# Kernel tuning notes

Measured on AMD Instinct MI355X. Metric: run time of the kernel, lower is better.

## Reference

```python
import jax, jax.numpy as jnp
import numpy as np

N = 16384
C = 128
F = 128

def setup_inputs() -> dict:
    key = jax.random.key(0)
    k1, k2, k3, k4 = jax.random.split(key, 4)
    X = jax.random.normal(k1, (N, C), dtype=jnp.float32)
    adj = jax.random.uniform(k2, (N, N), dtype=jnp.float32)
    W = jax.random.normal(k3, (C, F), dtype=jnp.float32) * 0.05
    b = jax.random.normal(k4, (F,), dtype=jnp.float32) * 0.05
    return {"X": X, "adj": adj, "W": W, "b": b}

def reference(X, adj, W, b):
    # adj_hat = adj + I (self-loops)
    adj_hat = adj + jnp.eye(adj.shape[0], dtype=adj.dtype)
    # D^{-1/2}: inverse of sqrt of the diagonal degree matrix == 1/sqrt(rowsum)
    d_inv_sqrt = 1.0 / jnp.sqrt(jnp.sum(adj_hat, axis=1))  # [N]
    # Symmetric normalization via row/col scaling (same math as D^-1/2 @ A @ D^-1/2)
    adj_norm = adj_hat * d_inv_sqrt[:, None] * d_inv_sqrt[None, :]
    # Feature transform first (N*C*F) then aggregate (N*N*F)
    out = adj_norm @ (X @ W) + b
    return jax.nn.relu(out)
```

## Files before the change

### kernel.cpp

```cpp
#include <hip/hip_runtime.h>
#include <hip/hip_bf16.h>

typedef __attribute__((ext_vector_type(8))) short short8;
typedef __attribute__((ext_vector_type(4))) float f32x4;

#define N_NODES 16384
#define FEAT 128

__device__ __forceinline__ short f2bf(float x) {
  union { float f; unsigned u; } v;
  v.f = x;
  unsigned r = v.u + 0x7fffu + ((v.u >> 16) & 1u);
  return (short)(r >> 16);
}

__global__ __launch_bounds__(256) void rowsum_kernel(
    const float* __restrict__ adj, float* __restrict__ dinv)
{
  const int row = blockIdx.x;
  const float4* p4 = (const float4*)(adj + (size_t)row * N_NODES);
  float s = 0.f;
  #pragma unroll 4
  for (int i = threadIdx.x; i < N_NODES / 4; i += 256) {
    float4 v = p4[i];
    s += (v.x + v.y) + (v.z + v.w);
  }
  #pragma unroll
  for (int off = 32; off > 0; off >>= 1) s += __shfl_down(s, off, 64);
  __shared__ float part[4];
  if ((threadIdx.x & 63) == 0) part[threadIdx.x >> 6] = s;
  __syncthreads();
  if (threadIdx.x == 0) {
    float tot = (part[0] + part[1]) + (part[2] + part[3]) + 1.0f;
    dinv[row] = rsqrtf(tot);
  }
}

__global__ __launch_bounds__(256) void xw_kernel(
    const float* __restrict__ X, const float* __restrict__ W,
    const float* __restrict__ dinv,
    __hip_bfloat16* __restrict__ Ynat, __hip_bfloat16* __restrict__ Ytg)
{
  __shared__ __align__(16) float Ws[64][128];
  __shared__ __align__(16) float Xs[32][128];
  __shared__ __align__(16) short Ts[128][40];
  const int tid = threadIdx.x;
  const int row0 = blockIdx.x << 5;

  {
    const float4* Xg = (const float4*)(X + ((size_t)row0 << 7));
    float4* Xl = (float4*)&Xs[0][0];
    #pragma unroll
    for (int i = 0; i < 4; ++i) Xl[tid + (i << 8)] = Xg[tid + (i << 8)];
  }
  const int f  = tid & 127;
  const int rr = tid >> 7;
  float acc[16];
  #pragma unroll
  for (int k = 0; k < 16; ++k) acc[k] = 0.f;

  for (int cc = 0; cc < 2; ++cc) {
    __syncthreads();
    {
      const float4* Wg = (const float4*)(W + ((size_t)cc << 13));
      float4* Wl = (float4*)&Ws[0][0];
      #pragma unroll
      for (int i = 0; i < 8; ++i) Wl[tid + (i << 8)] = Wg[tid + (i << 8)];
    }
    __syncthreads();
    for (int c4 = 0; c4 < 16; ++c4) {
      const int cl = c4 << 2;
      const float w0 = Ws[cl + 0][f];
      const float w1 = Ws[cl + 1][f];
      const float w2 = Ws[cl + 2][f];
      const float w3 = Ws[cl + 3][f];
      const int cg = (cc << 6) + cl;
      #pragma unroll
      for (int k = 0; k < 16; ++k) {
        const float4 x = *(const float4*)&Xs[rr + (k << 1)][cg];
        acc[k] += x.x * w0 + x.y * w1 + x.z * w2 + x.w * w3;
      }
    }
  }
  #pragma unroll
  for (int k = 0; k < 16; ++k) {
    const int r = rr + (k << 1);
    const float dv = dinv[row0 + r];
    const short v = f2bf(acc[k] * dv);
    ((short*)Ynat)[(size_t)(row0 + r) * FEAT + f] = v;
    Ts[f][r] = v;
  }
  __syncthreads();
  {
    const int f2 = tid >> 1;
    const int h  = (tid & 1) << 4;
    const short8 v0 = *(const short8*)&Ts[f2][h];
    const short8 v1 = *(const short8*)&Ts[f2][h + 8];
    short* o = (short*)Ytg + (size_t)f2 * N_NODES + row0 + h;
    *(short8*)(o)     = v0;
    *(short8*)(o + 8) = v1;
  }
}

__global__ __launch_bounds__(512) void spmm_kernel(
    const float* __restrict__ A,
    const __hip_bfloat16* __restrict__ Ynat,
    const __hip_bfloat16* __restrict__ Ytg,
    const float* __restrict__ dinv,
    const float* __restrict__ bias,
    float* __restrict__ out)
{
  __shared__ __align__(16) short As[2][64][72];
  __shared__ __align__(16) short Bs[2][128][72];
  const int tid  = threadIdx.x;
  const int row0 = blockIdx.x << 6;

  const int ar = tid >> 3;
  const int ak = (tid & 7) << 3;
  const float* Ag = A + (size_t)(row0 + ar) * N_NODES + ak;
  const int yf = tid >> 2;
  const int yk = (tid & 3) << 4;
  const short* Yg = (const short*)Ytg + (size_t)yf * N_NODES + yk;

  const int wid  = tid >> 6;
  const int wm   = wid >> 1;
  const int wf   = wid & 1;
  const int lane = tid & 63;
  const int lm   = lane & 15;
  const int lk   = (lane >> 4) << 3;

  f32x4 acc[4];
  #pragma unroll
  for (int c = 0; c < 4; ++c) acc[c] = (f32x4){0.f, 0.f, 0.f, 0.f};

  {
    const float4 a0 = *(const float4*)(Ag);
    const float4 a1 = *(const float4*)(Ag + 4);
    const short8 y0 = *(const short8*)(Yg);
    const short8 y1 = *(const short8*)(Yg + 8);
    short8 ac;
    ac[0] = f2bf(a0.x); ac[1] = f2bf(a0.y); ac[2] = f2bf(a0.z); ac[3] = f2bf(a0.w);
    ac[4] = f2bf(a1.x); ac[5] = f2bf(a1.y); ac[6] = f2bf(a1.z); ac[7] = f2bf(a1.w);
    *(short8*)&As[0][ar][ak]     = ac;
    *(short8*)&Bs[0][yf][yk]     = y0;
    *(short8*)&Bs[0][yf][yk + 8] = y1;
  }
  __syncthreads();

  int p = 0;
  for (int t = 0; t < N_NODES / 64; ++t) {
    float4 a0, a1; short8 y0, y1;
    const bool pre = (t + 1) < (N_NODES / 64);
    if (pre) {
      const float* Ab = Ag + ((size_t)(t + 1) << 6);
      a0 = *(const float4*)(Ab);
      a1 = *(const float4*)(Ab + 4);
      const short* Yb = Yg + ((t + 1) << 6);
      y0 = *(const short8*)(Yb);
      y1 = *(const short8*)(Yb + 8);
    }
    #pragma unroll
    for (int ks = 0; ks < 2; ++ks) {
      const short8 af = *(const short8*)&As[p][(wm << 4) + lm][(ks << 5) + lk];
      #pragma unroll
      for (int c = 0; c < 4; ++c) {
        const short8 bf = *(const short8*)&Bs[p][(wf << 6) + (c << 4) + lm][(ks << 5) + lk];
        acc[c] = __builtin_amdgcn_mfma_f32_16x16x32_bf16(af, bf, acc[c], 0, 0, 0);
      }
    }
    if (pre) {
      short8 ac;
      ac[0] = f2bf(a0.x); ac[1] = f2bf(a0.y); ac[2] = f2bf(a0.z); ac[3] = f2bf(a0.w);
      ac[4] = f2bf(a1.x); ac[5] = f2bf(a1.y); ac[6] = f2bf(a1.z); ac[7] = f2bf(a1.w);
      *(short8*)&As[p ^ 1][ar][ak]     = ac;
      *(short8*)&Bs[p ^ 1][yf][yk]     = y0;
      *(short8*)&Bs[p ^ 1][yf][yk + 8] = y1;
    }
    __syncthreads();
    p ^= 1;
  }

  const int lr = (lane >> 4) << 2;
  float dreg[4];
  #pragma unroll
  for (int r = 0; r < 4; ++r) dreg[r] = dinv[row0 + (wm << 4) + lr + r];
  #pragma unroll
  for (int c = 0; c < 4; ++c) {
    const int col = (wf << 6) + (c << 4) + lm;
    const float bv = bias[col];
    #pragma unroll
    for (int r = 0; r < 4; ++r) {
      const int row = row0 + (wm << 4) + lr + r;
      const float y = __bfloat162float(Ynat[(size_t)row * FEAT + col]);
      const float v = dreg[r] * (acc[c][r] + y) + bv;
      out[(size_t)row * FEAT + col] = v > 0.f ? v : 0.f;
    }
  }
}

extern "C" void kernel_launch(void* const* d_in, const int* in_sizes, int n_in,
                              void* d_out, int out_size, void* d_ws, size_t ws_size,
                              hipStream_t stream) {
  const float* X   = (const float*)d_in[0];
  const float* adj = (const float*)d_in[1];
  const float* W   = (const float*)d_in[2];
  const float* b   = (const float*)d_in[3];
  float* out = (float*)d_out;

  float* dinv = (float*)d_ws;
  __hip_bfloat16* Ynat = (__hip_bfloat16*)((char*)d_ws + (1 << 16));
  __hip_bfloat16* Ytg  = (__hip_bfloat16*)((char*)d_ws + (1 << 16) + (1 << 22));

  rowsum_kernel<<<N_NODES, 256, 0, stream>>>(adj, dinv);
  xw_kernel<<<N_NODES / 32, 256, 0, stream>>>(X, W, dinv, Ynat, Ytg);
  spmm_kernel<<<N_NODES / 64, 512, 0, stream>>>(adj, Ynat, Ytg, dinv, b, out);
}
```

Baseline: 478.0 us.

## Load Y fragments directly into registers from pre-packed layout, drop B LDS staging

xw_kernel now writes Y in a fragment-packed layout so each SpMM lane can load its MFMA B operands straight from global memory into registers, removing the Bs shared-memory tile and its LDS writes and reads. The SpMM loop is unrolled by two with ping-pong register buffers, A is prefetched two tiles ahead, and launch bounds request two blocks per CU. The cost is more registers per thread and duplicate global reads of Y across waves sharing the same wf, which L2 has to absorb.

Measured after the change: 487.4 us. Within noise of the previous version (+2.0%).

```diff
diff --git a/kernel.cpp b/kernel.cpp
--- a/kernel.cpp
+++ b/kernel.cpp
@@ -6,6 +6,7 @@
 
 #define N_NODES 16384
 #define FEAT 128
+#define NT 256
 
 __device__ __forceinline__ short f2bf(float x) {
   union { float f; unsigned u; } v;
@@ -39,7 +40,7 @@
 __global__ __launch_bounds__(256) void xw_kernel(
     const float* __restrict__ X, const float* __restrict__ W,
     const float* __restrict__ dinv,
-    __hip_bfloat16* __restrict__ Ynat, __hip_bfloat16* __restrict__ Ytg)
+    __hip_bfloat16* __restrict__ Ynat, __hip_bfloat16* __restrict__ Ypack)
 {
   __shared__ __align__(16) float Ws[64][128];
   __shared__ __align__(16) float Xs[32][128];
@@ -96,31 +97,69 @@
     const int h  = (tid & 1) << 4;
     const short8 v0 = *(const short8*)&Ts[f2][h];
     const short8 v1 = *(const short8*)&Ts[f2][h + 8];
-    short* o = (short*)Ytg + (size_t)f2 * N_NODES + row0 + h;
-    *(short8*)(o)     = v0;
-    *(short8*)(o + 8) = v1;
-  }
-}
-
-__global__ __launch_bounds__(512) void spmm_kernel(
+    short* o = (short*)Ypack;
+    *(short8*)(o + (size_t)(row0 + h) * FEAT + (f2 << 3))     = v0;
+    *(short8*)(o + (size_t)(row0 + h + 8) * FEAT + (f2 << 3)) = v1;
+  }
+}
+
+#define SPMM_BODY(T, BCUR, BNXT, ALD0, ALD1, AST0, AST1, RD, WR)               \
+  {                                                                            \
+    if ((T) + 2 < NT) {           \
+      const float* ap = Ag + (((T) + 2) << 6);                                 \
+      ALD0 = *(const float4*)(ap);                                             \
+      ALD1 = *(const float4*)(ap + 4);                                         \
+    }                                                                          \
+    if ((T) + 1 < NT) {  \
+      const short* yp0 = Yg + (((T) + 1) << 13);                               \
+      const short* yp1 = yp0 + 4096;                                           \
+      BNXT[0] = *(const short8*)(yp0);                                         \
+      BNXT[1] = *(const short8*)(yp0 + 128);                                   \
+      BNXT[2] = *(const short8*)(yp0 + 256);                                   \
+      BNXT[3] = *(const short8*)(yp0 + 384);                                   \
+      BNXT[4] = *(const short8*)(yp1);                                         \
+      BNXT[5] = *(const short8*)(yp1 + 128);                                   \
+      BNXT[6] = *(const short8*)(yp1 + 256);                                   \
+      BNXT[7] = *(const short8*)(yp1 + 384);                                   \
+    }                                                                          \
+    {                                                                          \
+      const short8 af0 = *(const short8*)&As[RD][(wm << 4) + lm][lk];          \
+      acc[0] = __builtin_amdgcn_mfma_f32_16x16x32_bf16(af0, BCUR[0], acc[0], 0, 0, 0); \
+      acc[1] = __builtin_amdgcn_mfma_f32_16x16x32_bf16(af0, BCUR[1], acc[1], 0, 0, 0); \
+      acc[2] = __builtin_amdgcn_mfma_f32_16x16x32_bf16(af0, BCUR[2], acc[2], 0, 0, 0); \
+      acc[3] = __builtin_amdgcn_mfma_f32_16x16x32_bf16(af0, BCUR[3], acc[3], 0, 0, 0); \
+      const short8 af1 = *(const short8*)&As[RD][(wm << 4) + lm][32 + lk];     \
+      acc[0] = __builtin_amdgcn_mfma_f32_16x16x32_bf16(af1, BCUR[4], acc[0], 0, 0, 0); \
+      acc[1] = __builtin_amdgcn_mfma_f32_16x16x32_bf16(af1, BCUR[5], acc[1], 0, 0, 0); \
+      acc[2] = __builtin_amdgcn_mfma_f32_16x16x32_bf16(af1, BCUR[6], acc[2], 0, 0, 0); \
+      acc[3] = __builtin_amdgcn_mfma_f32_16x16x32_bf16(af1, BCUR[7], acc[3], 0, 0, 0); \
+    }                                                                          \
+    if ((T) + 1 < NT) {  \
+      short8 ac;                                                               \
+      ac[0] = f2bf(AST0.x); ac[1] = f2bf(AST0.y);                              \
+      ac[2] = f2bf(AST0.z); ac[3] = f2bf(AST0.w);                              \
+      ac[4] = f2bf(AST1.x); ac[5] = f2bf(AST1.y);                              \
+      ac[6] = f2bf(AST1.z); ac[7] = f2bf(AST1.w);                              \
+      *(short8*)&As[WR][ar][ak] = ac;                                          \
+    }                                                                          \
+    __syncthreads();                                                           \
+  }
+
+__global__ __launch_bounds__(512, 2) void spmm_kernel(
     const float* __restrict__ A,
     const __hip_bfloat16* __restrict__ Ynat,
-    const __hip_bfloat16* __restrict__ Ytg,
+    const __hip_bfloat16* __restrict__ Ypack,
     const float* __restrict__ dinv,
     const float* __restrict__ bias,
     float* __restrict__ out)
 {
   __shared__ __align__(16) short As[2][64][72];
-  __shared__ __align__(16) short Bs[2][128][72];
   const int tid  = threadIdx.x;
   const int row0 = blockIdx.x << 6;
 
   const int ar = tid >> 3;
   const int ak = (tid & 7) << 3;
   const float* Ag = A + (size_t)(row0 + ar) * N_NODES + ak;
-  const int yf = tid >> 2;
-  const int yk = (tid & 3) << 4;
-  const short* Yg = (const short*)Ytg + (size_t)yf * N_NODES + yk;
 
   const int wid  = tid >> 6;
   const int wm   = wid >> 1;
@@ -129,55 +168,42 @@
   const int lm   = lane & 15;
   const int lk   = (lane >> 4) << 3;
 
+  const short* Yg = (const short*)Ypack + (lk << 7) + (wf << 9) + (lm << 3);
+
   f32x4 acc[4];
   #pragma unroll
   for (int c = 0; c < 4; ++c) acc[c] = (f32x4){0.f, 0.f, 0.f, 0.f};
 
-  {
-    const float4 a0 = *(const float4*)(Ag);
-    const float4 a1 = *(const float4*)(Ag + 4);
-    const short8 y0 = *(const short8*)(Yg);
-    const short8 y1 = *(const short8*)(Yg + 8);
+  float4 aA0, aA1, aB0, aB1;
+  short8 b0[8], b1[8];
+
+  aA0 = *(const float4*)(Ag);
+  aA1 = *(const float4*)(Ag + 4);
+  aB0 = *(const float4*)(Ag + 64);
+  aB1 = *(const float4*)(Ag + 68);
+  {
+    const short* yp0 = Yg;
+    const short* yp1 = Yg + 4096;
+    b0[0] = *(const short8*)(yp0);
+    b0[1] = *(const short8*)(yp0 + 128);
+    b0[2] = *(const short8*)(yp0 + 256);
+    b0[3] = *(const short8*)(yp0 + 384);
+    b0[4] = *(const short8*)(yp1);
+    b0[5] = *(const short8*)(yp1 + 128);
+    b0[6] = *(const short8*)(yp1 + 256);
+    b0[7] = *(const short8*)(yp1 + 384);
+  }
+  {
     short8 ac;
-    ac[0] = f2bf(a0.x); ac[1] = f2bf(a0.y); ac[2] = f2bf(a0.z); ac[3] = f2bf(a0.w);
-    ac[4] = f2bf(a1.x); ac[5] = f2bf(a1.y); ac[6] = f2bf(a1.z); ac[7] = f2bf(a1.w);
-    *(short8*)&As[0][ar][ak]     = ac;
-    *(short8*)&Bs[0][yf][yk]     = y0;
-    *(short8*)&Bs[0][yf][yk + 8] = y1;
+    ac[0] = f2bf(aA0.x); ac[1] = f2bf(aA0.y); ac[2] = f2bf(aA0.z); ac[3] = f2bf(aA0.w);
+    ac[4] = f2bf(aA1.x); ac[5] = f2bf(aA1.y); ac[6] = f2bf(aA1.z); ac[7] = f2bf(aA1.w);
+    *(short8*)&As[0][ar][ak] = ac;
   }
   __syncthreads();
 
-  int p = 0;
-  for (int t = 0; t < N_NODES / 64; ++t) {
-    float4 a0, a1; short8 y0, y1;
-    const bool pre = (t + 1) < (N_NODES / 64);
-    if (pre) {
-      const float* Ab = Ag + ((size_t)(t + 1) << 6);
-      a0 = *(const float4*)(Ab);
-      a1 = *(const float4*)(Ab + 4);
-      const short* Yb = Yg + ((t + 1) << 6);
-      y0 = *(const short8*)(Yb);
-      y1 = *(const short8*)(Yb + 8);
-    }
-    #pragma unroll
-    for (int ks = 0; ks < 2; ++ks) {
-      const short8 af = *(const short8*)&As[p][(wm << 4) + lm][(ks << 5) + lk];
-      #pragma unroll
-      for (int c = 0; c < 4; ++c) {
-        const short8 bf = *(const short8*)&Bs[p][(wf << 6) + (c << 4) + lm][(ks << 5) + lk];
-        acc[c] = __builtin_amdgcn_mfma_f32_16x16x32_bf16(af, bf, acc[c], 0, 0, 0);
-      }
-    }
-    if (pre) {
-      short8 ac;
-      ac[0] = f2bf(a0.x); ac[1] = f2bf(a0.y); ac[2] = f2bf(a0.z); ac[3] = f2bf(a0.w);
-      ac[4] = f2bf(a1.x); ac[5] = f2bf(a1.y); ac[6] = f2bf(a1.z); ac[7] = f2bf(a1.w);
-      *(short8*)&As[p ^ 1][ar][ak]     = ac;
-      *(short8*)&Bs[p ^ 1][yf][yk]     = y0;
-      *(short8*)&Bs[p ^ 1][yf][yk + 8] = y1;
-    }
-    __syncthreads();
-    p ^= 1;
+  for (int t = 0; t < NT; t += 2) {
+    SPMM_BODY(t,     b0, b1, aA0, aA1, aB0, aB1, 0, 1)
+    SPMM_BODY(t + 1, b1, b0, aB0, aB1, aA0, aA1, 1, 0)
   }
 
   const int lr = (lane >> 4) << 2;
@@ -208,10 +234,10 @@
   float* out = (float*)d_out;
 
   float* dinv = (float*)d_ws;
-  __hip_bfloat16* Ynat = (__hip_bfloat16*)((char*)d_ws + (1 << 16));
-  __hip_bfloat16* Ytg  = (__hip_bfloat16*)((char*)d_ws + (1 << 16) + (1 << 22));
+  __hip_bfloat16* Ynat  = (__hip_bfloat16*)((char*)d_ws + (1 << 16));
+  __hip_bfloat16* Ypack = (__hip_bfloat16*)((char*)d_ws + (1 << 16) + (1 << 22));
 
   rowsum_kernel<<<N_NODES, 256, 0, stream>>>(adj, dinv);
-  xw_kernel<<<N_NODES / 32, 256, 0, stream>>>(X, W, dinv, Ynat, Ytg);
-  spmm_kernel<<<N_NODES / 64, 512, 0, stream>>>(adj, Ynat, Ytg, dinv, b, out);
-}
+  xw_kernel<<<N_NODES / 32, 256, 0, stream>>>(X, W, dinv, Ynat, Ypack);
+  spmm_kernel<<<N_NODES / 64, 512, 0, stream>>>(adj, Ynat, Ypack, dinv, b, out);
+}
```

## Split-K the aggregation GEMM, pack Y layout, fold self-loop into A tile

Applied to the files above, without the earlier changes.

The dense aggregation is split across two K halves, so 512 blocks run instead of 256. Each block writes fp32 partial sums to workspace, and a new reduce kernel sums them and applies dinv, bias and ReLU. The Y matrix is stored in a packed k-group-major layout so global loads and LDS fragment reads are contiguous, and the self-loop identity is added into the A tile on the diagonal. The aim is more occupancy and better use of all CUs during the bandwidth-bound pass over adj. The cost is an extra kernel launch and 16 MB of partial-sum traffic.

Result: faster. 409.6 us (-14.3%).

```diff
diff --git a/kernel.cpp b/kernel.cpp
--- a/kernel.cpp
+++ b/kernel.cpp
@@ -6,6 +6,9 @@
 
 #define N_NODES 16384
 #define FEAT 128
+#define NTILES 256
+#define KSPLIT 2
+#define NT2 (NTILES / KSPLIT)
 
 __device__ __forceinline__ short f2bf(float x) {
   union { float f; unsigned u; } v;
@@ -39,7 +42,7 @@
 __global__ __launch_bounds__(256) void xw_kernel(
     const float* __restrict__ X, const float* __restrict__ W,
     const float* __restrict__ dinv,
-    __hip_bfloat16* __restrict__ Ynat, __hip_bfloat16* __restrict__ Ytg)
+    __hip_bfloat16* __restrict__ Ypack)
 {
   __shared__ __align__(16) float Ws[64][128];
   __shared__ __align__(16) float Xs[32][128];
@@ -86,9 +89,7 @@
   for (int k = 0; k < 16; ++k) {
     const int r = rr + (k << 1);
     const float dv = dinv[row0 + r];
-    const short v = f2bf(acc[k] * dv);
-    ((short*)Ynat)[(size_t)(row0 + r) * FEAT + f] = v;
-    Ts[f][r] = v;
+    Ts[f][r] = f2bf(acc[k] * dv);
   }
   __syncthreads();
   {
@@ -96,106 +97,145 @@
     const int h  = (tid & 1) << 4;
     const short8 v0 = *(const short8*)&Ts[f2][h];
     const short8 v1 = *(const short8*)&Ts[f2][h + 8];
-    short* o = (short*)Ytg + (size_t)f2 * N_NODES + row0 + h;
-    *(short8*)(o)     = v0;
-    *(short8*)(o + 8) = v1;
-  }
-}
-
-__global__ __launch_bounds__(512) void spmm_kernel(
+    short* o = (short*)Ypack;
+    *(short8*)(o + (size_t)(row0 + h) * FEAT + (f2 << 3))     = v0;
+    *(short8*)(o + (size_t)(row0 + h + 8) * FEAT + (f2 << 3)) = v1;
+  }
+}
+
+__global__ __launch_bounds__(512, 4) void spmm_kernel(
     const float* __restrict__ A,
-    const __hip_bfloat16* __restrict__ Ynat,
-    const __hip_bfloat16* __restrict__ Ytg,
-    const float* __restrict__ dinv,
-    const float* __restrict__ bias,
-    float* __restrict__ out)
-{
-  __shared__ __align__(16) short As[2][64][72];
-  __shared__ __align__(16) short Bs[2][128][72];
-  const int tid  = threadIdx.x;
-  const int row0 = blockIdx.x << 6;
-
-  const int ar = tid >> 3;
-  const int ak = (tid & 7) << 3;
-  const float* Ag = A + (size_t)(row0 + ar) * N_NODES + ak;
-  const int yf = tid >> 2;
-  const int yk = (tid & 3) << 4;
-  const short* Yg = (const short*)Ytg + (size_t)yf * N_NODES + yk;
+    const __hip_bfloat16* __restrict__ Ypack,
+    float* __restrict__ pws)
+{
+  __shared__ __align__(16) short As[2][4096];
+  __shared__ __align__(16) short Bs[2][8192];
+
+  const int tid = threadIdx.x;
+  const int bid = blockIdx.x;
+  const int mt  = bid & 255;
+  const int s   = bid >> 8;
+  const int row0 = mt << 6;
+
+  const int ar  = tid >> 3;
+  const int akg = tid & 7;
+  const float* Ag = A + (size_t)(row0 + ar) * N_NODES + (s * NT2 << 6) + (akg << 3);
+  const short* Yg = (const short*)Ypack + ((size_t)(s * NT2) << 13) + (tid << 4);
 
   const int wid  = tid >> 6;
   const int wm   = wid >> 1;
   const int wf   = wid & 1;
   const int lane = tid & 63;
   const int lm   = lane & 15;
-  const int lk   = (lane >> 4) << 3;
+  const int lkg  = (lane >> 4);
+  const int myrow = (wm << 4) + lm;
 
   f32x4 acc[4];
   #pragma unroll
   for (int c = 0; c < 4; ++c) acc[c] = (f32x4){0.f, 0.f, 0.f, 0.f};
 
-  {
-    const float4 a0 = *(const float4*)(Ag);
-    const float4 a1 = *(const float4*)(Ag + 4);
-    const short8 y0 = *(const short8*)(Yg);
-    const short8 y1 = *(const short8*)(Yg + 8);
-    short8 ac;
-    ac[0] = f2bf(a0.x); ac[1] = f2bf(a0.y); ac[2] = f2bf(a0.z); ac[3] = f2bf(a0.w);
-    ac[4] = f2bf(a1.x); ac[5] = f2bf(a1.y); ac[6] = f2bf(a1.z); ac[7] = f2bf(a1.w);
-    *(short8*)&As[0][ar][ak]     = ac;
-    *(short8*)&Bs[0][yf][yk]     = y0;
-    *(short8*)&Bs[0][yf][yk + 8] = y1;
-  }
+  float4 a0, a1;
+  short8 y0, y1;
+
+#define LOADT(T)                                                               \
+  {                                                                            \
+    const float* ap = Ag + ((T) << 6);                                         \
+    a0 = *(const float4*)(ap);                                                 \
+    a1 = *(const float4*)(ap + 4);                                             \
+    const short* yp = Yg + ((T) << 13);                                        \
+    y0 = *(const short8*)(yp);                                                 \
+    y1 = *(const short8*)(yp + 8);                                             \
+  }
+
+#define STORET(T, P)                                                           \
+  {                                                                            \
+    if (s * NT2 + (T) == mt && (ar >> 3) == akg) {          \
+      const int j = ar & 7;                                                    \
+      a0.x += (j == 0) ? 1.f : 0.f;  a0.y += (j == 1) ? 1.f : 0.f;             \
+      a0.z += (j == 2) ? 1.f : 0.f;  a0.w += (j == 3) ? 1.f : 0.f;             \
+      a1.x += (j == 4) ? 1.f : 0.f;  a1.y += (j == 5) ? 1.f : 0.f;             \
+      a1.z += (j == 6) ? 1.f : 0.f;  a1.w += (j == 7) ? 1.f : 0.f;             \
+    }                                                                          \
+    short8 av;                                                                 \
+    av[0] = f2bf(a0.x); av[1] = f2bf(a0.y); av[2] = f2bf(a0.z);                \
+    av[3] = f2bf(a0.w); av[4] = f2bf(a1.x); av[5] = f2bf(a1.y);                \
+    av[6] = f2bf(a1.z); av[7] = f2bf(a1.w);                                    \
+    *(short8*)&As[P][(akg << 9) + (ar << 3)] = av;                             \
+    *(short8*)&Bs[P][tid << 4]       = y0;                                     \
+    *(short8*)&Bs[P][(tid << 4) + 8] = y1;                                     \
+  }
+
+#define COMP(P)                                                                \
+  {                                                                            \
+    const short8 af0 = *(const short8*)&As[P][(lkg << 9) + (myrow << 3)];      \
+    acc[0] = __builtin_amdgcn_mfma_f32_16x16x32_bf16(af0,                      \
+        *(const short8*)&Bs[P][(lkg << 10) + (((wf << 6) + lm) << 3)], acc[0], 0, 0, 0); \
+    acc[1] = __builtin_amdgcn_mfma_f32_16x16x32_bf16(af0,                      \
+        *(const short8*)&Bs[P][(lkg << 10) + (((wf << 6) + 16 + lm) << 3)], acc[1], 0, 0, 0); \
+    acc[2] = __builtin_amdgcn_mfma_f32_16x16x32_bf16(af0,                      \
+        *(const short8*)&Bs[P][(lkg << 10) + (((wf << 6) + 32 + lm) << 3)], acc[2], 0, 0, 0); \
+    acc[3] = __builtin_amdgcn_mfma_f32_16x16x32_bf16(af0,                      \
+        *(const short8*)&Bs[P][(lkg << 10) + (((wf << 6) + 48 + lm) << 3)], acc[3], 0, 0, 0); \
+    const short8 af1 = *(const short8*)&As[P][((4 + lkg) << 9) + (myrow << 3)];\
+    acc[0] = __builtin_amdgcn_mfma_f32_16x16x32_bf16(af1,                      \
+        *(const short8*)&Bs[P][((4 + lkg) << 10) + (((wf << 6) + lm) << 3)], acc[0], 0, 0, 0); \
+    acc[1] = __builtin_amdgcn_mfma_f32_16x16x32_bf16(af1,                      \
+        *(const short8*)&Bs[P][((4 + lkg) << 10) + (((wf << 6) + 16 + lm) << 3)], acc[1], 0, 0, 0); \
+    acc[2] = __builtin_amdgcn_mfma_f32_16x16x32_bf16(af1,                      \
+        *(const short8*)&Bs[P][((4 + lkg) << 10) + (((wf << 6) + 32 + lm) << 3)], acc[2], 0, 0, 0); \
+    acc[3] = __builtin_amdgcn_mfma_f32_16x16x32_bf16(af1,                      \
+        *(const short8*)&Bs[P][((4 + lkg) << 10) + (((wf << 6) + 48 + lm) << 3)], acc[3], 0, 0, 0); \
+  }
+
+  LOADT(0)
+  STORET(0, 0)
   __syncthreads();
 
   int p = 0;
-  for (int t = 0; t < N_NODES / 64; ++t) {
-    float4 a0, a1; short8 y0, y1;
-    const bool pre = (t + 1) < (N_NODES / 64);
-    if (pre) {
-      const float* Ab = Ag + ((size_t)(t + 1) << 6);
-      a0 = *(const float4*)(Ab);
-      a1 = *(const float4*)(Ab + 4);
-      const short* Yb = Yg + ((t + 1) << 6);
-      y0 = *(const short8*)(Yb);
-      y1 = *(const short8*)(Yb + 8);
-    }
-    #pragma unroll
-    for (int ks = 0; ks < 2; ++ks) {
-      const short8 af = *(const short8*)&As[p][(wm << 4) + lm][(ks << 5) + lk];
-      #pragma unroll
-      for (int c = 0; c < 4; ++c) {
-        const short8 bf = *(const short8*)&Bs[p][(wf << 6) + (c << 4) + lm][(ks << 5) + lk];
-        acc[c] = __builtin_amdgcn_mfma_f32_16x16x32_bf16(af, bf, acc[c], 0, 0, 0);
-      }
-    }
-    if (pre) {
-      short8 ac;
-      ac[0] = f2bf(a0.x); ac[1] = f2bf(a0.y); ac[2] = f2bf(a0.z); ac[3] = f2bf(a0.w);
-      ac[4] = f2bf(a1.x); ac[5] = f2bf(a1.y); ac[6] = f2bf(a1.z); ac[7] = f2bf(a1.w);
-      *(short8*)&As[p ^ 1][ar][ak]     = ac;
-      *(short8*)&Bs[p ^ 1][yf][yk]     = y0;
-      *(short8*)&Bs[p ^ 1][yf][yk + 8] = y1;
-    }
+  for (int t = 0; t < NT2; ++t) {
+    if (t + 1 < NT2) LOADT(t + 1)
+    COMP(p)
+    if (t + 1 < NT2) STORET(t + 1, p ^ 1)
     __syncthreads();
     p ^= 1;
   }
 
+  float* pp = pws + ((size_t)(s * N_NODES + row0)) * FEAT;
   const int lr = (lane >> 4) << 2;
-  float dreg[4];
-  #pragma unroll
-  for (int r = 0; r < 4; ++r) dreg[r] = dinv[row0 + (wm << 4) + lr + r];
   #pragma unroll
   for (int c = 0; c < 4; ++c) {
     const int col = (wf << 6) + (c << 4) + lm;
-    const float bv = bias[col];
     #pragma unroll
     for (int r = 0; r < 4; ++r) {
-      const int row = row0 + (wm << 4) + lr + r;
-      const float y = __bfloat162float(Ynat[(size_t)row * FEAT + col]);
-      const float v = dreg[r] * (acc[c][r] + y) + bv;
-      out[(size_t)row * FEAT + col] = v > 0.f ? v : 0.f;
+      pp[(size_t)((wm << 4) + lr + r) * FEAT + col] = acc[c][r];
     }
   }
+#undef LOADT
+#undef STORET
+#undef COMP
+}
+
+__global__ __launch_bounds__(256) void reduce_kernel(
+    const float* __restrict__ pws, const float* __restrict__ dinv,
+    const float* __restrict__ bias, float* __restrict__ out)
+{
+  const int idx4 = blockIdx.x * 256 + threadIdx.x;
+  const int row  = idx4 >> 5;
+  const int f4   = idx4 & 31;
+  const float4 p0 = ((const float4*)pws)[idx4];
+  const float4 p1 = ((const float4*)pws)[idx4 + (N_NODES * FEAT / 4)];
+  const float4 bv = ((const float4*)bias)[f4];
+  const float  d  = dinv[row];
+  float4 v;
+  v.x = d * (p0.x + p1.x) + bv.x;
+  v.y = d * (p0.y + p1.y) + bv.y;
+  v.z = d * (p0.z + p1.z) + bv.z;
+  v.w = d * (p0.w + p1.w) + bv.w;
+  v.x = v.x > 0.f ? v.x : 0.f;
+  v.y = v.y > 0.f ? v.y : 0.f;
+  v.z = v.z > 0.f ? v.z : 0.f;
+  v.w = v.w > 0.f ? v.w : 0.f;
+  ((float4*)out)[idx4] = v;
 }
 
 extern "C" void kernel_launch(void* const* d_in, const int* in_sizes, int n_in,
@@ -207,11 +247,12 @@
   const float* b   = (const float*)d_in[3];
   float* out = (float*)d_out;
 
-  float* dinv = (float*)d_ws;
-  __hip_bfloat16* Ynat = (__hip_bfloat16*)((char*)d_ws + (1 << 16));
-  __hip_bfloat16* Ytg  = (__hip_bfloat16*)((char*)d_ws + (1 << 16) + (1 << 22));
+  float* dinv           = (float*)d_ws;
+  __hip_bfloat16* Ypack = (__hip_bfloat16*)((char*)d_ws + (1 << 16));
+  float* pws            = (float*)((char*)d_ws + (1 << 16) + (1 << 22));
 
   rowsum_kernel<<<N_NODES, 256, 0, stream>>>(adj, dinv);
-  xw_kernel<<<N_NODES / 32, 256, 0, stream>>>(X, W, dinv, Ynat, Ytg);
-  spmm_kernel<<<N_NODES / 64, 512, 0, stream>>>(adj, Ynat, Ytg, dinv, b, out);
-}
+  xw_kernel<<<N_NODES / 32, 256, 0, stream>>>(X, W, dinv, Ypack);
+  spmm_kernel<<<NTILES * KSPLIT, 512, 0, stream>>>(adj, Ypack, pws);
+  reduce_kernel<<<N_NODES * FEAT / 4 / 256, 256, 0, stream>>>(pws, dinv, b, out);
+}
```
